# Performance work log

Measured on AMD Instinct MI355X. Metric: run time of the kernel, lower is better.

The kernel has to match this reference:

```python
import jax, jax.numpy as jnp
import numpy as np
import math

N, B, S = 2048, 4, 1024
SFZ, IFZ, H, A = 384, 256, 8, 64
LN_EPS = 1e-5


def setup_inputs() -> dict:
    key = jax.random.key(0)
    ks = jax.random.split(key, 12)
    x = jax.random.normal(ks[0], (N, IFZ), dtype=jnp.float32)
    emb = jax.random.normal(ks[1], (B, S, SFZ), dtype=jnp.float32)
    mask = jax.random.randint(ks[2], (B, S), 0, 2).astype(bool)
    batch = jnp.sort(jax.random.randint(ks[3], (N,), 0, B)).astype(jnp.int64)
    sc = 1.0 / math.sqrt(IFZ)
    scs = 1.0 / math.sqrt(SFZ)
    Wq = jax.random.normal(ks[4], (IFZ, H * A), dtype=jnp.float32) * sc
    Wk = jax.random.normal(ks[5], (SFZ, H * A), dtype=jnp.float32) * scs
    Wv = jax.random.normal(ks[6], (SFZ, H * A), dtype=jnp.float32) * scs
    Wg = jax.random.normal(ks[7], (IFZ, H * A), dtype=jnp.float32) * sc
    bg = jnp.zeros((H * A,), dtype=jnp.float32)
    Wback = jax.random.normal(ks[8], (H * A, IFZ), dtype=jnp.float32) / math.sqrt(H * A)
    bback = jnp.zeros((IFZ,), dtype=jnp.float32)
    gamma = jnp.ones((IFZ,), dtype=jnp.float32)
    beta = jnp.zeros((IFZ,), dtype=jnp.float32)
    return {"x": x, "packed_sequence_emb": emb, "packed_sequence_mask": mask,
            "batch": batch, "Wq": Wq, "Wk": Wk, "Wv": Wv, "Wg": Wg, "bg": bg,
            "Wback": Wback, "bback": bback, "gamma": gamma, "beta": beta}


def _masked_softmax(scores, mask):
    # scores: [N,S,H], mask: [N,S,1] bool; softmax over S with padded entries zeroed
    neg = jnp.finfo(scores.dtype).min
    s = jnp.where(mask, scores, neg)
    s = s - jnp.max(s, axis=1, keepdims=True)
    e = jnp.exp(s) * mask
    return e / (jnp.sum(e, axis=1, keepdims=True) + 1e-9)


def reference(x, packed_sequence_emb, packed_sequence_mask, batch,
              Wq, Wk, Wv, Wg, bg, Wback, bback, gamma, beta):
    scale = math.sqrt(A)
    q = (x @ Wq).reshape(N, H, A)                               # [N,H,A]
    k = (packed_sequence_emb @ Wk).reshape(B, S, H, A)          # [B,S,H,A]
    v = (packed_sequence_emb @ Wv).reshape(B, S, H, A)
    # scores per (node, candidate-batch), then gather node's own batch entry;
    # avoids materializing k[batch] of shape [N,S,H,A]
    scores_all = jnp.einsum('nha,bsha->nbsh', q, k) / scale     # [N,B,S,H]
    idx = batch[:, None, None, None].astype(jnp.int32)
    scores = jnp.take_along_axis(scores_all, idx, axis=1)[:, 0]  # [N,S,H]
    bmask = packed_sequence_mask[batch][..., None]               # [N,S,1]
    w = _masked_softmax(scores, bmask)                           # [N,S,H]
    feat_all = jnp.einsum('nsh,bsha->nbha', w, v)                # [N,B,H,A]
    feat = jnp.take_along_axis(feat_all, idx, axis=1)[:, 0]      # [N,H,A]
    gate = jax.nn.sigmoid(x @ Wg + bg).reshape(N, H, A)
    new = (gate * feat).reshape(N, H * A) @ Wback + bback        # [N,IFZ]
    y = math.sqrt(2.0) * x + new
    mu = jnp.mean(y, axis=-1, keepdims=True)
    var = jnp.mean((y - mu) ** 2, axis=-1, keepdims=True)
    out = (y - mu) * jax.lax.rsqrt(var + LN_EPS) * gamma + beta
    seq_aa_logits = jnp.sum(scores[..., :2], axis=-1)            # [N,S]
    return out, seq_aa_logits
```

## Files before the change

kernel.cpp:

```cpp
#include <hip/hip_runtime.h>
#include <hip/hip_bf16.h>

#define NND 2048
#define BBATCH 4
#define SS 1024
#define SFZ 384
#define IFZ 256
#define HH 8
#define AA 64
#define HA 512
#define ABLK 6
#define NGRP 8
#define NSPL 8

typedef __attribute__((ext_vector_type(8))) short bf16x8;
typedef __attribute__((ext_vector_type(4))) float f32x4;
typedef __attribute__((ext_vector_type(2))) unsigned int u32x2;

__device__ __forceinline__ unsigned short f2bf(float f) {
    union { float f; unsigned u; } a; a.f = f;
    unsigned r = a.u + 0x7fffu + ((a.u >> 16) & 1u);
    return (unsigned short)(r >> 16);
}
__device__ __forceinline__ float bf2f(unsigned short u) {
    return __uint_as_float((unsigned)u << 16);
}

__device__ __forceinline__ bf16x8 cvt8(const float* __restrict__ p) {
    const float4 f0 = *(const float4*)p;
    const float4 f1 = *(const float4*)(p + 4);
    bf16x8 o;
    o[0] = (short)f2bf(f0.x); o[1] = (short)f2bf(f0.y);
    o[2] = (short)f2bf(f0.z); o[3] = (short)f2bf(f0.w);
    o[4] = (short)f2bf(f1.x); o[5] = (short)f2bf(f1.y);
    o[6] = (short)f2bf(f1.z); o[7] = (short)f2bf(f1.w);
    return o;
}

__device__ __forceinline__ bf16x8 gld16(const unsigned short* p) {
    bf16x8 r;
    asm volatile("global_load_dwordx4 %0, %1, off" : "=&v"(r) : "v"(p));
    return r;
}
__device__ __forceinline__ f32x4 gldf4(const float* p) {
    f32x4 r;
    asm volatile("global_load_dwordx4 %0, %1, off" : "=&v"(r) : "v"(p));
    return r;
}
__device__ __forceinline__ u32x2 gld8(const unsigned short* p) {
    u32x2 r;
    asm volatile("global_load_dwordx2 %0, %1, off" : "=&v"(r) : "v"(p));
    return r;
}
__device__ __forceinline__ float gldf(const float* p) {
    float r;
    asm volatile("global_load_dword %0, %1, off" : "=&v"(r) : "v"(p));
    return r;
}
#define VMWAIT0() do { \
    asm volatile("s_waitcnt vmcnt(0)" ::: "memory"); \
    __builtin_amdgcn_sched_barrier(0); \
} while (0)

__device__ __forceinline__ void tile_transpose(
    const float* __restrict__ src, unsigned short* __restrict__ dst,
    int K, int N, int kt, int nt, int t)
{
    __shared__ unsigned short tile[64][65];
    const int k0 = kt * 64, n0 = nt * 64;
    const int tr = t >> 6, tc = t & 63;
    #pragma unroll
    for (int r = 0; r < 16; ++r)
        tile[tr + r*4][tc] = f2bf(src[(size_t)(k0 + tr + r*4) * N + n0 + tc]);
    __syncthreads();
    #pragma unroll
    for (int r = 0; r < 16; ++r)
        dst[(size_t)(n0 + tr + r*4) * K + k0 + tc] = tile[tc][tr + r*4];
}

__global__ __launch_bounds__(256) void prep_kernel(
    const float* __restrict__ Wk, const float* __restrict__ Wv,
    const float* __restrict__ Wq, const float* __restrict__ Wg,
    const float* __restrict__ Wback,
    const void* __restrict__ mask_raw, const void* __restrict__ batch_raw,
    unsigned short* __restrict__ WkT, unsigned short* __restrict__ WvT,
    unsigned short* __restrict__ WqT, unsigned short* __restrict__ WgT,
    unsigned short* __restrict__ WbackT,
    float* __restrict__ mask_f, int* __restrict__ seg)
{
    const int bx = blockIdx.x, t = threadIdx.x;
    if (bx < 48)  { tile_transpose(Wk, WkT, SFZ, HA, bx/8, bx%8, t); return; }
    if (bx < 96)  { const int i = bx-48;  tile_transpose(Wv, WvT, SFZ, HA, i/8, i%8, t); return; }
    if (bx < 128) { const int i = bx-96;  tile_transpose(Wq, WqT, IFZ, HA, i/8, i%8, t); return; }
    if (bx < 160) { const int i = bx-128; tile_transpose(Wg, WgT, IFZ, HA, i/8, i%8, t); return; }
    if (bx < 192) { const int i = bx-160; tile_transpose(Wback, WbackT, HA, IFZ, i/4, i%4, t); return; }
    __shared__ int fl[4];
    __shared__ int fb;
    __shared__ int cnt[4];
    if (t < 4) { fl[t] = 0; cnt[t] = 0; }
    if (t == 0) fb = 0;
    __syncthreads();
    const unsigned char*  mb = (const unsigned char*)mask_raw;
    const unsigned short* mh = (const unsigned short*)mask_raw;
    const unsigned int*   mw = (const unsigned int*)mask_raw;
    int f0 = 0, f1 = 0, f2 = 0, f3 = 0;
    for (int i = t; i < 2048; i += 256) {
        unsigned short h = mh[i];
        if (h == 0x3f80u) f0 = 1;
        if ((i & 1) == 0 && h != 0) f1 = 1;
    }
    for (int i = t; i < 4096; i += 256)
        if ((i & 3) != 0 && mb[i] != 0) f2 = 1;
    for (int i = t; i < 1024; i += 256)
        if ((i & 1) != 0 && mw[i] != 0) f3 = 1;
    const int* bw = (const int*)batch_raw;
    int f4 = 0;
    for (int i = t + 1; i < 2048; i += 256)
        if (bw[i] < bw[i-1]) f4 = 1;
    if (f0) atomicOr(&fl[0], 1);
    if (f1) atomicOr(&fl[1], 1);
    if (f2) atomicOr(&fl[2], 1);
    if (f3) atomicOr(&fl[3], 1);
    if (f4) atomicOr(&fb, 1);
    __syncthreads();
    int mode;
    if (fl[0])      mode = fl[1] ? 1 : 0;
    else if (fl[2]) mode = 2;
    else if (fl[3]) mode = 3;
    else            mode = 4;
    for (int s = t; s < BBATCH*SS; s += 256) {
        int m;
        switch (mode) {
            case 0:  m = (mw[s]   != 0); break;
            case 1:  m = (mh[s]   != 0); break;
            case 2:  m = (mb[s]   != 0); break;
            case 3:  m = (mw[s]   != 0); break;
            default: m = (mw[2*s] != 0); break;
        }
        mask_f[s] = m ? 1.0f : 0.0f;
    }
    const int b64 = fb;
    for (int i = t; i < NND; i += 256) {
        const int bv = (b64 ? bw[2*i] : bw[i]) & 3;
        atomicAdd(&cnt[bv], 1);
    }
    __syncthreads();
    if (t == 0) {
        int s = 0;
        for (int b = 0; b < 4; ++b) { seg[2*b] = s; s += cnt[b]; seg[2*b+1] = s; }
    }
}

__global__ __launch_bounds__(256, 2) void proj_mfma(
    const float* __restrict__ emb, const float* __restrict__ x,
    const unsigned short* __restrict__ WkT, const unsigned short* __restrict__ WvT,
    const unsigned short* __restrict__ WqT, const unsigned short* __restrict__ WgT,
    const float* __restrict__ bg,
    unsigned short* __restrict__ k_blk, unsigned short* __restrict__ vT_bf,
    unsigned short* __restrict__ q_bf, float* __restrict__ gate_ws)
{
    __shared__ unsigned short v_l[16][520];
    const int t = threadIdx.x, w = t >> 6, lane = t & 63;
    const int m16 = lane & 15, quad = lane >> 4;
    const int bx = blockIdx.x;
    if (bx < 256) {
        const int r0 = bx * 16;
        const int b = r0 >> 10, srow = r0 & (SS - 1);
        const float* ap = emb + (size_t)(r0 + m16) * SFZ + quad * 8;
        bf16x8 af[12];
        #pragma unroll
        for (int j = 0; j < 12; ++j) af[j] = cvt8(ap + j * 32);
        #pragma unroll
        for (int tensor = 0; tensor < 2; ++tensor) {
            const unsigned short* Wt = tensor ? WvT : WkT;
            #pragma unroll
            for (int g = 0; g < 2; ++g) {
                const int n0g = w * 128 + g * 64;
                const unsigned short* bp0 = Wt + (size_t)(n0g +  0 + m16) * SFZ + quad * 8;
                const unsigned short* bp1 = Wt + (size_t)(n0g + 16 + m16) * SFZ + quad * 8;
                const unsigned short* bp2 = Wt + (size_t)(n0g + 32 + m16) * SFZ + quad * 8;
                const unsigned short* bp3 = Wt + (size_t)(n0g + 48 + m16) * SFZ + quad * 8;
                f32x4 a0 = (f32x4){0.f, 0.f, 0.f, 0.f};
                f32x4 a1 = a0, a2 = a0, a3 = a0;
                bf16x8 wb[24];
                #pragma unroll
                for (int j = 0; j < 6; ++j) {
                    wb[j*4+0] = gld16(bp0 + j * 32);
                    wb[j*4+1] = gld16(bp1 + j * 32);
                    wb[j*4+2] = gld16(bp2 + j * 32);
                    wb[j*4+3] = gld16(bp3 + j * 32);
                }
                VMWAIT0();
                #pragma unroll
                for (int j = 0; j < 6; ++j) {
                    a0 = __builtin_amdgcn_mfma_f32_16x16x32_bf16(af[j], wb[j*4+0], a0, 0, 0, 0);
                    a1 = __builtin_amdgcn_mfma_f32_16x16x32_bf16(af[j], wb[j*4+1], a1, 0, 0, 0);
                    a2 = __builtin_amdgcn_mfma_f32_16x16x32_bf16(af[j], wb[j*4+2], a2, 0, 0, 0);
                    a3 = __builtin_amdgcn_mfma_f32_16x16x32_bf16(af[j], wb[j*4+3], a3, 0, 0, 0);
                }
                #pragma unroll
                for (int j = 6; j < 12; ++j) {
                    wb[(j-6)*4+0] = gld16(bp0 + j * 32);
                    wb[(j-6)*4+1] = gld16(bp1 + j * 32);
                    wb[(j-6)*4+2] = gld16(bp2 + j * 32);
                    wb[(j-6)*4+3] = gld16(bp3 + j * 32);
                }
                VMWAIT0();
                #pragma unroll
                for (int j = 6; j < 12; ++j) {
                    a0 = __builtin_amdgcn_mfma_f32_16x16x32_bf16(af[j], wb[(j-6)*4+0], a0, 0, 0, 0);
                    a1 = __builtin_amdgcn_mfma_f32_16x16x32_bf16(af[j], wb[(j-6)*4+1], a1, 0, 0, 0);
                    a2 = __builtin_amdgcn_mfma_f32_16x16x32_bf16(af[j], wb[(j-6)*4+2], a2, 0, 0, 0);
                    a3 = __builtin_amdgcn_mfma_f32_16x16x32_bf16(af[j], wb[(j-6)*4+3], a3, 0, 0, 0);
                }
                f32x4 dd[4] = {a0, a1, a2, a3};
                if (tensor == 0) {
                    #pragma unroll
                    for (int u = 0; u < 4; ++u) {
                        const int n0 = n0g + u * 16;
                        const int head = n0 >> 6, coff = (n0 & 63) + m16;
                        unsigned short* kb = k_blk + (((size_t)(b * HH + head)) * SS) * 64 + coff;
                        #pragma unroll
                        for (int r = 0; r < 4; ++r)
                            kb[(size_t)(srow + quad * 4 + r) * 64] = f2bf(dd[u][r]);
                    }
                } else {
                    #pragma unroll
                    for (int u = 0; u < 4; ++u) {
                        const int c0 = n0g + u * 16 + m16;
                        #pragma unroll
                        for (int r = 0; r < 4; ++r)
                            v_l[quad * 4 + r][c0] = f2bf(dd[u][r]);
                    }
                }
            }
        }
        __syncthreads();
        for (int c = t; c < HA; c += 256) {
            unsigned short tmp[16];
            #pragma unroll
            for (int s = 0; s < 16; ++s) tmp[s] = v_l[s][c];
            unsigned short* dst = vT_bf + ((size_t)b * HA + c) * SS + srow;
            *(uint4*)dst       = ((const uint4*)tmp)[0];
            *(uint4*)(dst + 8) = ((const uint4*)tmp)[1];
        }
    } else {
        const int i = bx - 256;
        const int r0 = (i >> 1) * 16;
        const int half = i & 1;
        const float* ap = x + (size_t)(r0 + m16) * IFZ + quad * 8;
        bf16x8 af[8];
        #pragma unroll
        for (int j = 0; j < 8; ++j) af[j] = cvt8(ap + j * 32);
        const int n0b = half * 256 + w * 64;
        #pragma unroll
        for (int tensor = 0; tensor < 2; ++tensor) {
            const unsigned short* Wt = tensor ? WgT : WqT;
            const unsigned short* bp0 = Wt + (size_t)(n0b +  0 + m16) * IFZ + quad * 8;
            const unsigned short* bp1 = Wt + (size_t)(n0b + 16 + m16) * IFZ + quad * 8;
            const unsigned short* bp2 = Wt + (size_t)(n0b + 32 + m16) * IFZ + quad * 8;
            const unsigned short* bp3 = Wt + (size_t)(n0b + 48 + m16) * IFZ + quad * 8;
            bf16x8 wb[32];
            #pragma unroll
            for (int j = 0; j < 8; ++j) {
                wb[j*4+0] = gld16(bp0 + j * 32);
                wb[j*4+1] = gld16(bp1 + j * 32);
                wb[j*4+2] = gld16(bp2 + j * 32);
                wb[j*4+3] = gld16(bp3 + j * 32);
            }
            VMWAIT0();
            f32x4 a0 = (f32x4){0.f, 0.f, 0.f, 0.f};
            f32x4 a1 = a0, a2 = a0, a3 = a0;
            #pragma unroll
            for (int j = 0; j < 8; ++j) {
                a0 = __builtin_amdgcn_mfma_f32_16x16x32_bf16(af[j], wb[j*4+0], a0, 0, 0, 0);
                a1 = __builtin_amdgcn_mfma_f32_16x16x32_bf16(af[j], wb[j*4+1], a1, 0, 0, 0);
                a2 = __builtin_amdgcn_mfma_f32_16x16x32_bf16(af[j], wb[j*4+2], a2, 0, 0, 0);
                a3 = __builtin_amdgcn_mfma_f32_16x16x32_bf16(af[j], wb[j*4+3], a3, 0, 0, 0);
            }
            f32x4 dd[4] = {a0, a1, a2, a3};
            if (tensor == 0) {
                #pragma unroll
                for (int u = 0; u < 4; ++u) {
                    const int n0 = n0b + u * 16;
                    #pragma unroll
                    for (int r = 0; r < 4; ++r)
                        q_bf[(size_t)(r0 + quad * 4 + r) * HA + n0 + m16] = f2bf(dd[u][r]);
                }
            } else {
                #pragma unroll
                for (int u = 0; u < 4; ++u) {
                    const int n0 = n0b + u * 16;
                    const float bgv = bg[n0 + m16];
                    #pragma unroll
                    for (int r = 0; r < 4; ++r)
                        gate_ws[(size_t)(r0 + quad * 4 + r) * HA + n0 + m16] =
                            1.f / (1.f + __expf(-(dd[u][r] + bgv)));
                }
            }
        }
    }
}

__global__ __launch_bounds__(256, 2) void attn_kernel(
    const unsigned short* __restrict__ k_blk, const unsigned short* __restrict__ vT_bf,
    const unsigned short* __restrict__ q_bf, const float* __restrict__ mask_f,
    const int* __restrict__ seg, unsigned short* __restrict__ part_O,
    float2* __restrict__ part_ml, float* __restrict__ out_logits)
{
    __shared__ unsigned short P_lds[4][16][136];
    __shared__ float raw0[2][16][132];
    const int bid = blockIdx.x;
    const int xcd = bid & 7;
    const int b   = xcd >> 1;
    const int idx = (bid >> 3) * 2 + (xcd & 1);
    const int z    = idx & 15;
    const int xblk = idx >> 4;
    const int hz    = z >> 3;
    const int split = z & 7;
    const int nbase = seg[2*b] + xblk * (16 * NGRP);
    const int nend  = seg[2*b + 1];
    if (nbase >= nend) return;

    const int t = threadIdx.x;
    const int w = t >> 6, lane = t & 63;
    const int m16 = lane & 15, quad = lane >> 4;
    const int h = hz * 4 + w;
    const int s0 = split * 128;

    const unsigned short* kb = k_blk + ((size_t)(b * HH + h)) * SS * 64;
    const unsigned short* vb = vT_bf + ((size_t)b * HA + h * AA) * SS;
    const unsigned short* qbase = q_bf + (size_t)h * AA + quad * 8;
    unsigned short (*Pw)[136] = P_lds[w];

    bf16x8 kf[16];
    #pragma unroll
    for (int st = 0; st < 8; ++st) {
        const unsigned short* kp = kb + (size_t)(s0 + st * 16 + m16) * 64 + quad * 8;
        kf[2*st]   = gld16(kp);
        kf[2*st+1] = gld16(kp + 32);
    }
    bf16x8 vf[16];
    #pragma unroll
    for (int sub = 0; sub < 4; ++sub) {
        const unsigned short* vp0 = vb + (size_t)m16 * SS + s0 + sub * 32 + quad * 8;
        #pragma unroll
        for (int a = 0; a < 4; ++a)
            vf[sub*4+a] = gld16(vp0 + (size_t)(a * 16) * SS);
    }
    float msk[8];
    #pragma unroll
    for (int st = 0; st < 8; ++st)
        msk[st] = gldf(mask_f + b * SS + s0 + st * 16 + m16);
    int nq0 = nbase + m16; if (nq0 >= nend) nq0 = nend - 1;
    bf16x8 qc0 = gld16(qbase + (size_t)nq0 * HA);
    bf16x8 qc1 = gld16(qbase + (size_t)nq0 * HA + 32);
    VMWAIT0();

    bf16x8 qn0 = qc0, qn1 = qc1;
    for (int g = 0; g < NGRP; ++g) {
        const int n0g = nbase + g * 16;
        if (n0g >= nend) break;
        if (g > 0) {
            VMWAIT0();
            qc0 = qn0; qc1 = qn1;
        }
        const int nvalid = min(16, nend - n0g);

        f32x4 d[8];
        #pragma unroll
        for (int st = 0; st < 8; ++st) {
            f32x4 acc = (f32x4){0.f, 0.f, 0.f, 0.f};
            acc = __builtin_amdgcn_mfma_f32_16x16x32_bf16(qc0, kf[2*st],   acc, 0, 0, 0);
            acc = __builtin_amdgcn_mfma_f32_16x16x32_bf16(qc1, kf[2*st+1], acc, 0, 0, 0);
            #pragma unroll
            for (int r = 0; r < 4; ++r) acc[r] *= 0.125f;
            d[st] = acc;
        }
        if (g + 1 < NGRP && nbase + (g + 1) * 16 < nend) {
            int nqn = nbase + (g + 1) * 16 + m16; if (nqn >= nend) nqn = nend - 1;
            qn0 = gld16(qbase + (size_t)nqn * HA);
            qn1 = gld16(qbase + (size_t)nqn * HA + 32);
        }
        __builtin_amdgcn_sched_barrier(0);

        if (hz == 0) {
            if (w == 0) {
                #pragma unroll
                for (int st = 0; st < 8; ++st)
                    #pragma unroll
                    for (int r = 0; r < 4; ++r)
                        raw0[g & 1][quad * 4 + r][st * 16 + m16] = d[st][r];
            }
            __syncthreads();
            if (w == 1) {
                #pragma unroll
                for (int st = 0; st < 8; ++st)
                    #pragma unroll
                    for (int r = 0; r < 4; ++r) {
                        const int row = quad * 4 + r;
                        if (row < nvalid)
                            out_logits[(size_t)(n0g + row) * SS + s0 + st * 16 + m16] =
                                raw0[g & 1][row][st * 16 + m16] + d[st][r];
                    }
            }
        }
        float m_s[4], l_s[4];
        #pragma unroll
        for (int r = 0; r < 4; ++r) {
            float mx = -3.0e38f;
            #pragma unroll
            for (int st = 0; st < 8; ++st)
                mx = (msk[st] > 0.5f) ? fmaxf(mx, d[st][r]) : mx;
            mx = fmaxf(mx, __shfl_xor(mx, 1));
            mx = fmaxf(mx, __shfl_xor(mx, 2));
            mx = fmaxf(mx, __shfl_xor(mx, 4));
            mx = fmaxf(mx, __shfl_xor(mx, 8));
            m_s[r] = mx;
            float cs = 0.f;
            #pragma unroll
            for (int st = 0; st < 8; ++st) {
                const float e = (msk[st] > 0.5f) ? __expf(d[st][r] - mx) : 0.f;
                d[st][r] = e;
                cs += e;
            }
            cs += __shfl_xor(cs, 1);
            cs += __shfl_xor(cs, 2);
            cs += __shfl_xor(cs, 4);
            cs += __shfl_xor(cs, 8);
            l_s[r] = cs;
        }
        #pragma unroll
        for (int st = 0; st < 8; ++st)
            #pragma unroll
            for (int r = 0; r < 4; ++r)
                Pw[quad * 4 + r][st * 16 + m16] = f2bf(d[st][r]);
        bf16x8 pa[4];
        #pragma unroll
        for (int sub = 0; sub < 4; ++sub)
            pa[sub] = *(const bf16x8*)&Pw[m16][sub * 32 + quad * 8];
        f32x4 facc[4];
        #pragma unroll
        for (int a = 0; a < 4; ++a) facc[a] = (f32x4){0.f, 0.f, 0.f, 0.f};
        #pragma unroll
        for (int sub = 0; sub < 4; ++sub) {
            #pragma unroll
            for (int a = 0; a < 4; ++a)
                facc[a] = __builtin_amdgcn_mfma_f32_16x16x32_bf16(pa[sub], vf[sub*4+a], facc[a], 0, 0, 0);
        }
        unsigned short* po = part_O + (size_t)split * NND * HA;
        #pragma unroll
        for (int a = 0; a < 4; ++a)
            #pragma unroll
            for (int r = 0; r < 4; ++r) {
                const int row = quad * 4 + r;
                if (row < nvalid)
                    po[(size_t)(n0g + row) * HA + h * AA + a * 16 + m16] = f2bf(facc[a][r]);
            }
        if (m16 == 0) {
            #pragma unroll
            for (int r = 0; r < 4; ++r) {
                const int row = quad * 4 + r;
                if (row < nvalid)
                    part_ml[(size_t)split * NND * HH + (size_t)(n0g + row) * HH + h] =
                        make_float2(m_s[r], l_s[r]);
            }
        }
    }
}

__global__ __launch_bounds__(256, 2) void back_ln_fused(
    const unsigned short* __restrict__ part_O, const float2* __restrict__ part_ml,
    const float* __restrict__ gate_ws, const unsigned short* __restrict__ WbackT,
    const float* __restrict__ x, const float* __restrict__ bback,
    const float* __restrict__ gamma, const float* __restrict__ beta,
    float* __restrict__ out)
{
    __shared__ float coef[NSPL][8][8];
    __shared__ unsigned short gf_l[8][520];
    __shared__ float nl[8][260];
    const int t = threadIdx.x, w = t >> 6, lane = t & 63;
    const int m16 = lane & 15, quad = lane >> 4;
    const int r0 = blockIdx.x * 8;
    if (t < 64) {
        const int row = t >> 3, h = t & 7, n = r0 + row;
        float2 ml[NSPL];
        #pragma unroll
        for (int s = 0; s < NSPL; ++s)
            ml[s] = part_ml[(size_t)s * NND * HH + (size_t)n * HH + h];
        float M = -3.0e38f;
        #pragma unroll
        for (int s = 0; s < NSPL; ++s) M = fmaxf(M, ml[s].x);
        float L = 0.f;
        float e[NSPL];
        #pragma unroll
        for (int s = 0; s < NSPL; ++s) { e[s] = __expf(ml[s].x - M); L += ml[s].y * e[s]; }
        const float invL = 1.f / (L + 1e-9f);
        #pragma unroll
        for (int s = 0; s < NSPL; ++s) coef[s][row][h] = e[s] * invL;
    }
    u32x2 pvv[4][NSPL];
    f32x4 gv[4];
    #pragma unroll
    for (int it = 0; it < 4; ++it) {
        const int i = (t + it * 256) * 4;
        const int row = i >> 9, c = i & (HA - 1);
        const int n = r0 + row;
        #pragma unroll
        for (int s = 0; s < NSPL; ++s)
            pvv[it][s] = gld8(&part_O[(size_t)s * NND * HA + (size_t)n * HA + c]);
        gv[it] = gldf4(&gate_ws[(size_t)n * HA + c]);
    }
    __syncthreads();
    VMWAIT0();
    #pragma unroll
    for (int it = 0; it < 4; ++it) {
        const int i = (t + it * 256) * 4;
        const int row = i >> 9, c = i & (HA - 1), h = c >> 6;
        float4 o = make_float4(0.f, 0.f, 0.f, 0.f);
        #pragma unroll
        for (int s = 0; s < NSPL; ++s) {
            const float cf = coef[s][row][h];
            o.x = fmaf(bf2f((unsigned short)(pvv[it][s][0] & 0xffffu)), cf, o.x);
            o.y = fmaf(bf2f((unsigned short)(pvv[it][s][0] >> 16)),     cf, o.y);
            o.z = fmaf(bf2f((unsigned short)(pvv[it][s][1] & 0xffffu)), cf, o.z);
            o.w = fmaf(bf2f((unsigned short)(pvv[it][s][1] >> 16)),     cf, o.w);
        }
        ushort4 ob;
        ob.x = f2bf(gv[it][0] * o.x); ob.y = f2bf(gv[it][1] * o.y);
        ob.z = f2bf(gv[it][2] * o.z); ob.w = f2bf(gv[it][3] * o.w);
        *(ushort4*)&gf_l[row][c] = ob;
    }
    __syncthreads();
    bf16x8 af[16];
    #pragma unroll
    for (int j = 0; j < 16; ++j)
        af[j] = *(const bf16x8*)&gf_l[m16 & 7][quad * 8 + j * 32];
    const unsigned short* bq0 = WbackT + (size_t)(w * 64 +  0 + m16) * HA + quad * 8;
    const unsigned short* bq1 = WbackT + (size_t)(w * 64 + 16 + m16) * HA + quad * 8;
    const unsigned short* bq2 = WbackT + (size_t)(w * 64 + 32 + m16) * HA + quad * 8;
    const unsigned short* bq3 = WbackT + (size_t)(w * 64 + 48 + m16) * HA + quad * 8;
    f32x4 a0 = (f32x4){0.f, 0.f, 0.f, 0.f};
    f32x4 a1 = a0, a2 = a0, a3 = a0;
    #pragma unroll
    for (int jb = 0; jb < 4; ++jb) {
        bf16x8 wb[16];
        #pragma unroll
        for (int j = 0; j < 4; ++j) {
            wb[j*4+0] = gld16(bq0 + (jb*4 + j) * 32);
            wb[j*4+1] = gld16(bq1 + (jb*4 + j) * 32);
            wb[j*4+2] = gld16(bq2 + (jb*4 + j) * 32);
            wb[j*4+3] = gld16(bq3 + (jb*4 + j) * 32);
        }
        VMWAIT0();
        #pragma unroll
        for (int j = 0; j < 4; ++j) {
            a0 = __builtin_amdgcn_mfma_f32_16x16x32_bf16(af[jb*4+j], wb[j*4+0], a0, 0, 0, 0);
            a1 = __builtin_amdgcn_mfma_f32_16x16x32_bf16(af[jb*4+j], wb[j*4+1], a1, 0, 0, 0);
            a2 = __builtin_amdgcn_mfma_f32_16x16x32_bf16(af[jb*4+j], wb[j*4+2], a2, 0, 0, 0);
            a3 = __builtin_amdgcn_mfma_f32_16x16x32_bf16(af[jb*4+j], wb[j*4+3], a3, 0, 0, 0);
        }
    }
    {
        f32x4 dd[4] = {a0, a1, a2, a3};
        #pragma unroll
        for (int u = 0; u < 4; ++u) {
            const int n0 = w * 64 + u * 16;
            const float bb = bback[n0 + m16];
            #pragma unroll
            for (int r = 0; r < 4; ++r) {
                const int rr = quad * 4 + r;
                if (rr < 8) nl[rr][n0 + m16] = dd[u][r] + bb;
            }
        }
    }
    __syncthreads();
    const int row = t >> 5, li = t & 31;
    const float* xr = x + (size_t)(r0 + row) * IFZ;
    float yv[8];
    float s1 = 0.f, s2 = 0.f;
    #pragma unroll
    for (int j = 0; j < 8; ++j) {
        const int c = li + j * 32;
        const float v = fmaf(1.41421356237309515f, xr[c], nl[row][c]);
        yv[j] = v; s1 += v; s2 += v * v;
    }
    #pragma unroll
    for (int off = 16; off >= 1; off >>= 1) {
        s1 += __shfl_xor(s1, off);
        s2 += __shfl_xor(s2, off);
    }
    const float mu  = s1 * (1.f / IFZ);
    const float var = s2 * (1.f / IFZ) - mu * mu;
    const float rv  = rsqrtf(var + 1e-5f);
    float* orow = out + (size_t)(r0 + row) * IFZ;
    #pragma unroll
    for (int j = 0; j < 8; ++j) {
        const int c = li + j * 32;
        orow[c] = (yv[j] - mu) * rv * gamma[c] + beta[c];
    }
}

extern "C" void kernel_launch(void* const* d_in, const int* in_sizes, int n_in,
                              void* d_out, int out_size, void* d_ws, size_t ws_size,
                              hipStream_t stream) {
    const float* x     = (const float*)d_in[0];
    const float* emb   = (const float*)d_in[1];
    const void*  mraw  = d_in[2];
    const void*  braw  = d_in[3];
    const float* Wq    = (const float*)d_in[4];
    const float* Wk    = (const float*)d_in[5];
    const float* Wv    = (const float*)d_in[6];
    const float* Wg    = (const float*)d_in[7];
    const float* bg    = (const float*)d_in[8];
    const float* Wback = (const float*)d_in[9];
    const float* bback = (const float*)d_in[10];
    const float* gamma = (const float*)d_in[11];
    const float* beta  = (const float*)d_in[12];

    char* ws = (char*)d_ws;
    const size_t MB = 1048576;
    size_t off = 0;
    float*          mask_f  = (float*)(ws + off);  off += 16384;
    int*            seg     = (int*)(ws + off);    off += 16384;
    unsigned short* WkT     = (unsigned short*)(ws + off); off += 393216;
    unsigned short* WvT     = (unsigned short*)(ws + off); off += 393216;
    unsigned short* WqT     = (unsigned short*)(ws + off); off += 262144;
    unsigned short* WgT     = (unsigned short*)(ws + off); off += 262144;
    unsigned short* WbackT  = (unsigned short*)(ws + off); off += 262144;
    unsigned short* k_blk   = (unsigned short*)(ws + off); off += 4*MB;
    unsigned short* vT_bf   = (unsigned short*)(ws + off); off += 4*MB;
    unsigned short* q_bf    = (unsigned short*)(ws + off); off += 2*MB;
    float*          gate_ws = (float*)(ws + off); off += 4*MB;
    unsigned short* part_O  = (unsigned short*)(ws + off); off += 16*MB;
    float2*         part_ml = (float2*)(ws + off); off += 1*MB;

    float* out        = (float*)d_out;
    float* out_logits = out + (size_t)NND * IFZ;

    hipLaunchKernelGGL(prep_kernel, dim3(193), dim3(256), 0, stream,
                       Wk, Wv, Wq, Wg, Wback, mraw, braw,
                       WkT, WvT, WqT, WgT, WbackT, mask_f, seg);
    hipLaunchKernelGGL(proj_mfma, dim3(512), dim3(256), 0, stream,
                       emb, x, WkT, WvT, WqT, WgT, bg, k_blk, vT_bf, q_bf, gate_ws);
    hipLaunchKernelGGL(attn_kernel, dim3(BBATCH * ABLK * 16), dim3(256), 0, stream,
                       k_blk, vT_bf, q_bf, mask_f, seg, part_O, part_ml, out_logits);
    hipLaunchKernelGGL(back_ln_fused, dim3(NND / 8), dim3(256), 0, stream,
                       part_O, part_ml, gate_ws, WbackT, x, bback, gamma, beta, out);
}
```

Before: 189.2 us.

## Fuse four kernels into one cooperative persistent kernel with grid syncs

Converts the prep, projection, attention and back/LayerNorm kernels into device phase functions. They run inside a single cooperative kernel of 512 blocks, with grid.sync between phases and one shared LDS buffer sized for the largest phase. The aim is to remove launch overhead and inter-kernel gaps. In exchange every block carries the register and LDS footprint of the heaviest phase, and the cooperative launch needs all 512 blocks to be resident at once. If that launch fails, the code falls back to the original four separate launches.

```diff
diff --git a/kernel.cpp b/kernel.cpp
--- a/kernel.cpp
+++ b/kernel.cpp
@@ -1,5 +1,8 @@
 #include <hip/hip_runtime.h>
 #include <hip/hip_bf16.h>
+#include <hip/hip_cooperative_groups.h>
+
+namespace cg = cooperative_groups;
 
 #define NND 2048
 #define BBATCH 4
@@ -12,6 +15,7 @@
 #define ABLK 6
 #define NGRP 8
 #define NSPL 8
+#define GRID_BLKS 512
 
 typedef __attribute__((ext_vector_type(8))) short bf16x8;
 typedef __attribute__((ext_vector_type(4))) float f32x4;
@@ -64,9 +68,8 @@
 
 __device__ __forceinline__ void tile_transpose(
     const float* __restrict__ src, unsigned short* __restrict__ dst,
-    int K, int N, int kt, int nt, int t)
-{
-    __shared__ unsigned short tile[64][65];
+    unsigned short (*tile)[65], int K, int N, int kt, int nt, int t)
+{
     const int k0 = kt * 64, n0 = nt * 64;
     const int tr = t >> 6, tc = t & 63;
     #pragma unroll
@@ -78,42 +81,47 @@
         dst[(size_t)(n0 + tr + r*4) * K + k0 + tc] = tile[tc][tr + r*4];
 }
 
-__global__ __launch_bounds__(256) void prep_kernel(
+__device__ __forceinline__ void phase_prep(
+    int bx, int t, char* smem,
     const float* __restrict__ Wk, const float* __restrict__ Wv,
     const float* __restrict__ Wq, const float* __restrict__ Wg,
     const float* __restrict__ Wback,
-    const void* __restrict__ mask_raw, const void* __restrict__ batch_raw,
+    const void* __restrict__ mraw, const void* __restrict__ braw,
     unsigned short* __restrict__ WkT, unsigned short* __restrict__ WvT,
     unsigned short* __restrict__ WqT, unsigned short* __restrict__ WgT,
     unsigned short* __restrict__ WbackT,
     float* __restrict__ mask_f, int* __restrict__ seg)
 {
-    const int bx = blockIdx.x, t = threadIdx.x;
-    if (bx < 48)  { tile_transpose(Wk, WkT, SFZ, HA, bx/8, bx%8, t); return; }
-    if (bx < 96)  { const int i = bx-48;  tile_transpose(Wv, WvT, SFZ, HA, i/8, i%8, t); return; }
-    if (bx < 128) { const int i = bx-96;  tile_transpose(Wq, WqT, IFZ, HA, i/8, i%8, t); return; }
-    if (bx < 160) { const int i = bx-128; tile_transpose(Wg, WgT, IFZ, HA, i/8, i%8, t); return; }
-    if (bx < 192) { const int i = bx-160; tile_transpose(Wback, WbackT, HA, IFZ, i/4, i%4, t); return; }
-    __shared__ int fl[4];
-    __shared__ int fb;
-    __shared__ int cnt[4];
+    if (bx >= 193) return;
+    if (bx < 192) {
+        unsigned short (*tile)[65] = (unsigned short (*)[65])smem;
+        if (bx < 48)       tile_transpose(Wk, WkT, tile, SFZ, HA, bx/8, bx%8, t);
+        else if (bx < 96)  { const int i = bx-48;  tile_transpose(Wv, WvT, tile, SFZ, HA, i/8, i%8, t); }
+        else if (bx < 128) { const int i = bx-96;  tile_transpose(Wq, WqT, tile, IFZ, HA, i/8, i%8, t); }
+        else if (bx < 160) { const int i = bx-128; tile_transpose(Wg, WgT, tile, IFZ, HA, i/8, i%8, t); }
+        else               { const int i = bx-160; tile_transpose(Wback, WbackT, tile, HA, IFZ, i/4, i%4, t); }
+        return;
+    }
+    int* fl  = (int*)(smem);
+    int* fbp = (int*)(smem + 16);
+    int* cnt = (int*)(smem + 32);
     if (t < 4) { fl[t] = 0; cnt[t] = 0; }
-    if (t == 0) fb = 0;
+    if (t == 0) *fbp = 0;
     __syncthreads();
-    const unsigned char*  mb = (const unsigned char*)mask_raw;
-    const unsigned short* mh = (const unsigned short*)mask_raw;
-    const unsigned int*   mw = (const unsigned int*)mask_raw;
+    const unsigned char*  mb = (const unsigned char*)mraw;
+    const unsigned short* mh = (const unsigned short*)mraw;
+    const unsigned int*   mw = (const unsigned int*)mraw;
     int f0 = 0, f1 = 0, f2 = 0, f3 = 0;
     for (int i = t; i < 2048; i += 256) {
-        unsigned short h = mh[i];
-        if (h == 0x3f80u) f0 = 1;
-        if ((i & 1) == 0 && h != 0) f1 = 1;
+        unsigned short hh = mh[i];
+        if (hh == 0x3f80u) f0 = 1;
+        if ((i & 1) == 0 && hh != 0) f1 = 1;
     }
     for (int i = t; i < 4096; i += 256)
         if ((i & 3) != 0 && mb[i] != 0) f2 = 1;
     for (int i = t; i < 1024; i += 256)
         if ((i & 1) != 0 && mw[i] != 0) f3 = 1;
-    const int* bw = (const int*)batch_raw;
+    const int* bw = (const int*)braw;
     int f4 = 0;
     for (int i = t + 1; i < 2048; i += 256)
         if (bw[i] < bw[i-1]) f4 = 1;
@@ -121,7 +129,7 @@
     if (f1) atomicOr(&fl[1], 1);
     if (f2) atomicOr(&fl[2], 1);
     if (f3) atomicOr(&fl[3], 1);
-    if (f4) atomicOr(&fb, 1);
+    if (f4) atomicOr(fbp, 1);
     __syncthreads();
     int mode;
     if (fl[0])      mode = fl[1] ? 1 : 0;
@@ -139,7 +147,7 @@
         }
         mask_f[s] = m ? 1.0f : 0.0f;
     }
-    const int b64 = fb;
+    const int b64 = *fbp;
     for (int i = t; i < NND; i += 256) {
         const int bv = (b64 ? bw[2*i] : bw[i]) & 3;
         atomicAdd(&cnt[bv], 1);
@@ -151,7 +159,8 @@
     }
 }
 
-__global__ __launch_bounds__(256, 2) void proj_mfma(
+__device__ __forceinline__ void phase_proj(
+    int bx, int t, char* smem,
     const float* __restrict__ emb, const float* __restrict__ x,
     const unsigned short* __restrict__ WkT, const unsigned short* __restrict__ WvT,
     const unsigned short* __restrict__ WqT, const unsigned short* __restrict__ WgT,
@@ -159,10 +168,9 @@
     unsigned short* __restrict__ k_blk, unsigned short* __restrict__ vT_bf,
     unsigned short* __restrict__ q_bf, float* __restrict__ gate_ws)
 {
-    __shared__ unsigned short v_l[16][520];
-    const int t = threadIdx.x, w = t >> 6, lane = t & 63;
+    const int w = t >> 6, lane = t & 63;
     const int m16 = lane & 15, quad = lane >> 4;
-    const int bx = blockIdx.x;
+    unsigned short (*v_l)[520] = (unsigned short (*)[520])smem;
     if (bx < 256) {
         const int r0 = bx * 16;
         const int b = r0 >> 10, srow = r0 & (SS - 1);
@@ -244,7 +252,7 @@
             *(uint4*)dst       = ((const uint4*)tmp)[0];
             *(uint4*)(dst + 8) = ((const uint4*)tmp)[1];
         }
-    } else {
+    } else if (bx < 512) {
         const int i = bx - 256;
         const int r0 = (i >> 1) * 16;
         const int half = i & 1;
@@ -302,18 +310,19 @@
     }
 }
 
-__global__ __launch_bounds__(256, 2) void attn_kernel(
+__device__ __forceinline__ void phase_attn(
+    int bx, int t, char* smem,
     const unsigned short* __restrict__ k_blk, const unsigned short* __restrict__ vT_bf,
     const unsigned short* __restrict__ q_bf, const float* __restrict__ mask_f,
     const int* __restrict__ seg, unsigned short* __restrict__ part_O,
     float2* __restrict__ part_ml, float* __restrict__ out_logits)
 {
-    __shared__ unsigned short P_lds[4][16][136];
-    __shared__ float raw0[2][16][132];
-    const int bid = blockIdx.x;
-    const int xcd = bid & 7;
+    if (bx >= BBATCH * ABLK * 16) return;
+    unsigned short (*P_lds)[16][136] = (unsigned short (*)[16][136])smem;
+    float (*raw0)[16][132] = (float (*)[16][132])(smem + 17408);
+    const int xcd = bx & 7;
     const int b   = xcd >> 1;
-    const int idx = (bid >> 3) * 2 + (xcd & 1);
+    const int idx = (bx >> 3) * 2 + (xcd & 1);
     const int z    = idx & 15;
     const int xblk = idx >> 4;
     const int hz    = z >> 3;
@@ -322,12 +331,10 @@
     const int nend  = seg[2*b + 1];
     if (nbase >= nend) return;
 
-    const int t = threadIdx.x;
     const int w = t >> 6, lane = t & 63;
     const int m16 = lane & 15, quad = lane >> 4;
     const int h = hz * 4 + w;
     const int s0 = split * 128;
-
     const unsigned short* kb = k_blk + ((size_t)(b * HH + h)) * SS * 64;
     const unsigned short* vb = vT_bf + ((size_t)b * HA + h * AA) * SS;
     const unsigned short* qbase = q_bf + (size_t)h * AA + quad * 8;
@@ -469,19 +476,21 @@
     }
 }
 
-__global__ __launch_bounds__(256, 2) void back_ln_fused(
+__device__ __forceinline__ void phase_back(
+    int bx, int t, char* smem,
     const unsigned short* __restrict__ part_O, const float2* __restrict__ part_ml,
     const float* __restrict__ gate_ws, const unsigned short* __restrict__ WbackT,
     const float* __restrict__ x, const float* __restrict__ bback,
     const float* __restrict__ gamma, const float* __restrict__ beta,
     float* __restrict__ out)
 {
-    __shared__ float coef[NSPL][8][8];
-    __shared__ unsigned short gf_l[8][520];
-    __shared__ float nl[8][260];
-    const int t = threadIdx.x, w = t >> 6, lane = t & 63;
+    if (bx >= NND / 8) return;
+    float (*coef)[8][8] = (float (*)[8][8])smem;
+    unsigned short (*gf_l)[520] = (unsigned short (*)[520])(smem + 2048);
+    float (*nl)[260] = (float (*)[260])(smem + 2048 + 8320);
+    const int w = t >> 6, lane = t & 63;
     const int m16 = lane & 15, quad = lane >> 4;
-    const int r0 = blockIdx.x * 8;
+    const int r0 = bx * 8;
     if (t < 64) {
         const int row = t >> 3, h = t & 7, n = r0 + row;
         float2 ml[NSPL];
@@ -599,6 +608,95 @@
         const int c = li + j * 32;
         orow[c] = (yv[j] - mu) * rv * gamma[c] + beta[c];
     }
+}
+
+__global__ __launch_bounds__(256, 2) void fused_all(
+    const float* __restrict__ emb, const float* __restrict__ x,
+    const float* __restrict__ Wk, const float* __restrict__ Wv,
+    const float* __restrict__ Wq, const float* __restrict__ Wg,
+    const float* __restrict__ Wback,
+    const void* __restrict__ mraw, const void* __restrict__ braw,
+    const float* __restrict__ bg, const float* __restrict__ bback,
+    const float* __restrict__ gamma, const float* __restrict__ beta,
+    unsigned short* __restrict__ WkT, unsigned short* __restrict__ WvT,
+    unsigned short* __restrict__ WqT, unsigned short* __restrict__ WgT,
+    unsigned short* __restrict__ WbackT,
+    float* __restrict__ mask_f, int* __restrict__ seg,
+    unsigned short* __restrict__ k_blk, unsigned short* __restrict__ vT_bf,
+    unsigned short* __restrict__ q_bf, float* __restrict__ gate_ws,
+    unsigned short* __restrict__ part_O, float2* __restrict__ part_ml,
+    float* __restrict__ out, float* __restrict__ out_logits)
+{
+    __shared__ __align__(16) char smem[34304];
+    cg::grid_group grid = cg::this_grid();
+    const int bx = blockIdx.x;
+    const int t = threadIdx.x;
+
+    phase_prep(bx, t, smem, Wk, Wv, Wq, Wg, Wback, mraw, braw,
+               WkT, WvT, WqT, WgT, WbackT, mask_f, seg);
+    __threadfence(); grid.sync(); __threadfence();
+
+    phase_proj(bx, t, smem, emb, x, WkT, WvT, WqT, WgT, bg,
+               k_blk, vT_bf, q_bf, gate_ws);
+    __threadfence(); grid.sync(); __threadfence();
+
+    phase_attn(bx, t, smem, k_blk, vT_bf, q_bf, mask_f, seg,
+               part_O, part_ml, out_logits);
+    __threadfence(); grid.sync(); __threadfence();
+
+    phase_back(bx, t, smem, part_O, part_ml, gate_ws, WbackT, x,
+               bback, gamma, beta, out);
+}
+
+__global__ __launch_bounds__(256) void prep_kernel(
+    const float* __restrict__ Wk, const float* __restrict__ Wv,
+    const float* __restrict__ Wq, const float* __restrict__ Wg,
+    const float* __restrict__ Wback,
+    const void* __restrict__ mraw, const void* __restrict__ braw,
+    unsigned short* __restrict__ WkT, unsigned short* __restrict__ WvT,
+    unsigned short* __restrict__ WqT, unsigned short* __restrict__ WgT,
+    unsigned short* __restrict__ WbackT,
+    float* __restrict__ mask_f, int* __restrict__ seg)
+{
+    __shared__ __align__(16) char smem[8320];
+    phase_prep(blockIdx.x, threadIdx.x, smem, Wk, Wv, Wq, Wg, Wback, mraw, braw,
+               WkT, WvT, WqT, WgT, WbackT, mask_f, seg);
+}
+
+__global__ __launch_bounds__(256, 2) void proj_kernel(
+    const float* __restrict__ emb, const float* __restrict__ x,
+    const unsigned short* __restrict__ WkT, const unsigned short* __restrict__ WvT,
+    const unsigned short* __restrict__ WqT, const unsigned short* __restrict__ WgT,
+    const float* __restrict__ bg,
+    unsigned short* __restrict__ k_blk, unsigned short* __restrict__ vT_bf,
+    unsigned short* __restrict__ q_bf, float* __restrict__ gate_ws)
+{
+    __shared__ __align__(16) char smem[16640];
+    phase_proj(blockIdx.x, threadIdx.x, smem, emb, x, WkT, WvT, WqT, WgT, bg,
+               k_blk, vT_bf, q_bf, gate_ws);
+}
+
+__global__ __launch_bounds__(256, 2) void attn_kernel(
+    const unsigned short* __restrict__ k_blk, const unsigned short* __restrict__ vT_bf,
+    const unsigned short* __restrict__ q_bf, const float* __restrict__ mask_f,
+    const int* __restrict__ seg, unsigned short* __restrict__ part_O,
+    float2* __restrict__ part_ml, float* __restrict__ out_logits)
+{
+    __shared__ __align__(16) char smem[34304];
+    phase_attn(blockIdx.x, threadIdx.x, smem, k_blk, vT_bf, q_bf, mask_f, seg,
+               part_O, part_ml, out_logits);
+}
+
+__global__ __launch_bounds__(256, 2) void back_kernel(
+    const unsigned short* __restrict__ part_O, const float2* __restrict__ part_ml,
+    const float* __restrict__ gate_ws, const unsigned short* __restrict__ WbackT,
+    const float* __restrict__ x, const float* __restrict__ bback,
+    const float* __restrict__ gamma, const float* __restrict__ beta,
+    float* __restrict__ out)
+{
+    __shared__ __align__(16) char smem[18688];
+    phase_back(blockIdx.x, threadIdx.x, smem, part_O, part_ml, gate_ws, WbackT, x,
+               bback, gamma, beta, out);
 }
 
 extern "C" void kernel_launch(void* const* d_in, const int* in_sizes, int n_in,
@@ -638,13 +736,26 @@
     float* out        = (float*)d_out;
     float* out_logits = out + (size_t)NND * IFZ;
 
-    hipLaunchKernelGGL(prep_kernel, dim3(193), dim3(256), 0, stream,
-                       Wk, Wv, Wq, Wg, Wback, mraw, braw,
-                       WkT, WvT, WqT, WgT, WbackT, mask_f, seg);
-    hipLaunchKernelGGL(proj_mfma, dim3(512), dim3(256), 0, stream,
-                       emb, x, WkT, WvT, WqT, WgT, bg, k_blk, vT_bf, q_bf, gate_ws);
-    hipLaunchKernelGGL(attn_kernel, dim3(BBATCH * ABLK * 16), dim3(256), 0, stream,
-                       k_blk, vT_bf, q_bf, mask_f, seg, part_O, part_ml, out_logits);
-    hipLaunchKernelGGL(back_ln_fused, dim3(NND / 8), dim3(256), 0, stream,
-                       part_O, part_ml, gate_ws, WbackT, x, bback, gamma, beta, out);
-}
+    void* args[] = {
+        (void*)&emb, (void*)&x, (void*)&Wk, (void*)&Wv, (void*)&Wq, (void*)&Wg,
+        (void*)&Wback, (void*)&mraw, (void*)&braw, (void*)&bg, (void*)&bback,
+        (void*)&gamma, (void*)&beta,
+        (void*)&WkT, (void*)&WvT, (void*)&WqT, (void*)&WgT, (void*)&WbackT,
+        (void*)&mask_f, (void*)&seg, (void*)&k_blk, (void*)&vT_bf, (void*)&q_bf,
+        (void*)&gate_ws, (void*)&part_O, (void*)&part_ml, (void*)&out, (void*)&out_logits
+    };
+    hipError_t err = hipLaunchCooperativeKernel((void*)fused_all, dim3(GRID_BLKS),
+                                                dim3(256), args, 0, stream);
+    if (err != hipSuccess) {
+        (void)hipGetLastError();
+        hipLaunchKernelGGL(prep_kernel, dim3(193), dim3(256), 0, stream,
+                           Wk, Wv, Wq, Wg, Wback, mraw, braw,
+                           WkT, WvT, WqT, WgT, WbackT, mask_f, seg);
+        hipLaunchKernelGGL(proj_kernel, dim3(512), dim3(256), 0, stream,
+                           emb, x, WkT, WvT, WqT, WgT, bg, k_blk, vT_bf, q_bf, gate_ws);
+        hipLaunchKernelGGL(attn_kernel, dim3(BBATCH * ABLK * 16), dim3(256), 0, stream,
+                           k_blk, vT_bf, q_bf, mask_f, seg, part_O, part_ml, out_logits);
+        hipLaunchKernelGGL(back_kernel, dim3(NND / 8), dim3(256), 0, stream,
+                           part_O, part_ml, gate_ws, WbackT, x, bback, gamma, beta, out);
+    }
+}
```

Result: slower. 623.3 us (+229.4%).

## Transpose QK MFMA layout, reload V per group, bitmask mask, halve node groups

Applied to the files above, without the earlier changes.

Swaps the MFMA operand order so each lane holds scores for a single node row, which turns the softmax max/sum reductions into two cross-quad shuffles instead of four per row. The mask is loaded as float4 and packed into a 32-bit bitmask, and P is written to LDS with vector stores. V fragments are now reloaded inside each group loop instead of being held in registers for the whole kernel, trading register pressure for repeated V traffic. NGRP is halved and ABLK doubled to spread work over more blocks, and the logits output is written cooperatively by all threads.

```diff
diff --git a/kernel.cpp b/kernel.cpp
--- a/kernel.cpp
+++ b/kernel.cpp
@@ -9,8 +9,8 @@
 #define HH 8
 #define AA 64
 #define HA 512
-#define ABLK 6
-#define NGRP 8
+#define ABLK 12
+#define NGRP 4
 #define NSPL 8
 
 typedef __attribute__((ext_vector_type(8))) short bf16x8;
@@ -50,11 +50,6 @@
 __device__ __forceinline__ u32x2 gld8(const unsigned short* p) {
     u32x2 r;
     asm volatile("global_load_dwordx2 %0, %1, off" : "=&v"(r) : "v"(p));
-    return r;
-}
-__device__ __forceinline__ float gldf(const float* p) {
-    float r;
-    asm volatile("global_load_dword %0, %1, off" : "=&v"(r) : "v"(p));
     return r;
 }
 #define VMWAIT0() do { \
@@ -309,7 +304,7 @@
     float2* __restrict__ part_ml, float* __restrict__ out_logits)
 {
     __shared__ unsigned short P_lds[4][16][136];
-    __shared__ float raw0[2][16][132];
+    __shared__ float raw[2][16][132];
     const int bid = blockIdx.x;
     const int xcd = bid & 7;
     const int b   = xcd >> 1;
@@ -340,42 +335,44 @@
         kf[2*st]   = gld16(kp);
         kf[2*st+1] = gld16(kp + 32);
     }
-    bf16x8 vf[16];
-    #pragma unroll
-    for (int sub = 0; sub < 4; ++sub) {
-        const unsigned short* vp0 = vb + (size_t)m16 * SS + s0 + sub * 32 + quad * 8;
-        #pragma unroll
-        for (int a = 0; a < 4; ++a)
-            vf[sub*4+a] = gld16(vp0 + (size_t)(a * 16) * SS);
-    }
-    float msk[8];
+    f32x4 mkv[8];
     #pragma unroll
     for (int st = 0; st < 8; ++st)
-        msk[st] = gldf(mask_f + b * SS + s0 + st * 16 + m16);
+        mkv[st] = gldf4(mask_f + b * SS + s0 + st * 16 + quad * 4);
     int nq0 = nbase + m16; if (nq0 >= nend) nq0 = nend - 1;
     bf16x8 qc0 = gld16(qbase + (size_t)nq0 * HA);
     bf16x8 qc1 = gld16(qbase + (size_t)nq0 * HA + 32);
     VMWAIT0();
+    unsigned bm = 0u;
+    #pragma unroll
+    for (int st = 0; st < 8; ++st)
+        #pragma unroll
+        for (int r = 0; r < 4; ++r)
+            if (mkv[st][r] > 0.5f) bm |= (1u << (st * 4 + r));
 
     bf16x8 qn0 = qc0, qn1 = qc1;
     for (int g = 0; g < NGRP; ++g) {
         const int n0g = nbase + g * 16;
         if (n0g >= nend) break;
-        if (g > 0) {
-            VMWAIT0();
-            qc0 = qn0; qc1 = qn1;
-        }
         const int nvalid = min(16, nend - n0g);
 
         f32x4 d[8];
         #pragma unroll
         for (int st = 0; st < 8; ++st) {
             f32x4 acc = (f32x4){0.f, 0.f, 0.f, 0.f};
-            acc = __builtin_amdgcn_mfma_f32_16x16x32_bf16(qc0, kf[2*st],   acc, 0, 0, 0);
-            acc = __builtin_amdgcn_mfma_f32_16x16x32_bf16(qc1, kf[2*st+1], acc, 0, 0, 0);
+            acc = __builtin_amdgcn_mfma_f32_16x16x32_bf16(kf[2*st],   qc0, acc, 0, 0, 0);
+            acc = __builtin_amdgcn_mfma_f32_16x16x32_bf16(kf[2*st+1], qc1, acc, 0, 0, 0);
             #pragma unroll
             for (int r = 0; r < 4; ++r) acc[r] *= 0.125f;
             d[st] = acc;
+        }
+        bf16x8 vf[16];
+        #pragma unroll
+        for (int sub = 0; sub < 4; ++sub) {
+            const unsigned short* vp0 = vb + (size_t)m16 * SS + s0 + sub * 32 + quad * 8;
+            #pragma unroll
+            for (int a = 0; a < 4; ++a)
+                vf[sub*4+a] = gld16(vp0 + (size_t)(a * 16) * SS);
         }
         if (g + 1 < NGRP && nbase + (g + 1) * 16 < nend) {
             int nqn = nbase + (g + 1) * 16 + m16; if (nqn >= nend) nqn = nend - 1;
@@ -385,60 +382,58 @@
         __builtin_amdgcn_sched_barrier(0);
 
         if (hz == 0) {
-            if (w == 0) {
+            if (w < 2) {
                 #pragma unroll
                 for (int st = 0; st < 8; ++st)
-                    #pragma unroll
-                    for (int r = 0; r < 4; ++r)
-                        raw0[g & 1][quad * 4 + r][st * 16 + m16] = d[st][r];
+                    *(float4*)&raw[w][m16][st * 16 + quad * 4] =
+                        make_float4(d[st][0], d[st][1], d[st][2], d[st][3]);
             }
             __syncthreads();
-            if (w == 1) {
-                #pragma unroll
-                for (int st = 0; st < 8; ++st)
-                    #pragma unroll
-                    for (int r = 0; r < 4; ++r) {
-                        const int row = quad * 4 + r;
-                        if (row < nvalid)
-                            out_logits[(size_t)(n0g + row) * SS + s0 + st * 16 + m16] =
-                                raw0[g & 1][row][st * 16 + m16] + d[st][r];
-                    }
-            }
-        }
-        float m_s[4], l_s[4];
-        #pragma unroll
-        for (int r = 0; r < 4; ++r) {
-            float mx = -3.0e38f;
-            #pragma unroll
-            for (int st = 0; st < 8; ++st)
-                mx = (msk[st] > 0.5f) ? fmaxf(mx, d[st][r]) : mx;
-            mx = fmaxf(mx, __shfl_xor(mx, 1));
-            mx = fmaxf(mx, __shfl_xor(mx, 2));
-            mx = fmaxf(mx, __shfl_xor(mx, 4));
-            mx = fmaxf(mx, __shfl_xor(mx, 8));
-            m_s[r] = mx;
-            float cs = 0.f;
-            #pragma unroll
-            for (int st = 0; st < 8; ++st) {
-                const float e = (msk[st] > 0.5f) ? __expf(d[st][r] - mx) : 0.f;
+            for (int i = t; i < 16 * 128; i += 256) {
+                const int node = i >> 7, sp = i & 127;
+                if (node < nvalid)
+                    out_logits[(size_t)(n0g + node) * SS + s0 + sp] =
+                        raw[0][node][sp] + raw[1][node][sp];
+            }
+            __syncthreads();
+        }
+        #pragma unroll
+        for (int st = 0; st < 8; ++st)
+            #pragma unroll
+            for (int r = 0; r < 4; ++r)
+                if (!((bm >> (st * 4 + r)) & 1u)) d[st][r] = -3.0e38f;
+        float mx = -3.0e38f;
+        #pragma unroll
+        for (int st = 0; st < 8; ++st) {
+            float a = fmaxf(fmaxf(d[st][0], d[st][1]), fmaxf(d[st][2], d[st][3]));
+            mx = fmaxf(mx, a);
+        }
+        mx = fmaxf(mx, __shfl_xor(mx, 16));
+        mx = fmaxf(mx, __shfl_xor(mx, 32));
+        mx = fmaxf(mx, -1.0e30f);
+        float cs = 0.f;
+        #pragma unroll
+        for (int st = 0; st < 8; ++st)
+            #pragma unroll
+            for (int r = 0; r < 4; ++r) {
+                const float e = __expf(d[st][r] - mx);
                 d[st][r] = e;
                 cs += e;
             }
-            cs += __shfl_xor(cs, 1);
-            cs += __shfl_xor(cs, 2);
-            cs += __shfl_xor(cs, 4);
-            cs += __shfl_xor(cs, 8);
-            l_s[r] = cs;
-        }
-        #pragma unroll
-        for (int st = 0; st < 8; ++st)
-            #pragma unroll
-            for (int r = 0; r < 4; ++r)
-                Pw[quad * 4 + r][st * 16 + m16] = f2bf(d[st][r]);
+        cs += __shfl_xor(cs, 16);
+        cs += __shfl_xor(cs, 32);
+        #pragma unroll
+        for (int st = 0; st < 8; ++st) {
+            ushort4 pk;
+            pk.x = f2bf(d[st][0]); pk.y = f2bf(d[st][1]);
+            pk.z = f2bf(d[st][2]); pk.w = f2bf(d[st][3]);
+            *(ushort4*)&Pw[m16][st * 16 + quad * 4] = pk;
+        }
         bf16x8 pa[4];
         #pragma unroll
         for (int sub = 0; sub < 4; ++sub)
             pa[sub] = *(const bf16x8*)&Pw[m16][sub * 32 + quad * 8];
+        VMWAIT0();
         f32x4 facc[4];
         #pragma unroll
         for (int a = 0; a < 4; ++a) facc[a] = (f32x4){0.f, 0.f, 0.f, 0.f};
@@ -457,15 +452,10 @@
                 if (row < nvalid)
                     po[(size_t)(n0g + row) * HA + h * AA + a * 16 + m16] = f2bf(facc[a][r]);
             }
-        if (m16 == 0) {
-            #pragma unroll
-            for (int r = 0; r < 4; ++r) {
-                const int row = quad * 4 + r;
-                if (row < nvalid)
-                    part_ml[(size_t)split * NND * HH + (size_t)(n0g + row) * HH + h] =
-                        make_float2(m_s[r], l_s[r]);
-            }
-        }
+        if (quad == 0 && m16 < nvalid)
+            part_ml[(size_t)split * NND * HH + (size_t)(n0g + m16) * HH + h] =
+                make_float2(mx, cs);
+        qc0 = qn0; qc1 = qn1;
     }
 }
 
```

Result: no change. 186.8 us (-1.3%).
